# Optimization experiments

Measured on AMD Instinct MI355X. Metric: run time of the kernel, lower is better.

The kernel has to match this reference:

```python
import jax, jax.numpy as jnp
import numpy as np
from jax import lax


def ternarize(w):
    # TWN-style ternarization: threshold delta = 0.7*mean|w|, scale alpha =
    # mean |w| over surviving entries; straight-through in backward.
    aw = jnp.abs(w)
    delta = 0.7 * jnp.mean(aw)
    mask = (aw > delta).astype(w.dtype)
    alpha = jnp.sum(aw * mask) / jnp.maximum(jnp.sum(mask), 1.0)
    q = alpha * jnp.sign(w) * mask
    return w + lax.stop_gradient(q - w)


def conv2d(x, w, b):
    # x: [N,C,H,W], w: [O,I,kh,kw]
    y = lax.conv_general_dilated(x, w, window_strides=(1, 1), padding='VALID',
                                 dimension_numbers=('NCHW', 'OIHW', 'NCHW'))
    return y + b[None, :, None, None]


def maxpool2(x):
    return lax.reduce_window(x, -jnp.inf, lax.max,
                             window_dimensions=(1, 1, 2, 2),
                             window_strides=(1, 1, 2, 2), padding='VALID')


def setup_inputs() -> dict:
    key = jax.random.key(0)
    ks = jax.random.split(key, 11)
    n_classes = 10
    x = jax.random.normal(ks[0], (1024, 1, 32, 32), dtype=jnp.float32)
    # Kaiming-ish scaled params
    w1 = jax.random.normal(ks[1], (32, 1, 5, 5), jnp.float32) * (1.0 / np.sqrt(1 * 25))
    b1 = jnp.zeros((32,), jnp.float32)
    w2 = jax.random.normal(ks[2], (64, 32, 5, 5), jnp.float32) * (1.0 / np.sqrt(32 * 25))
    b2 = jnp.zeros((64,), jnp.float32)
    w3 = jax.random.normal(ks[3], (120, 64, 5, 5), jnp.float32) * (1.0 / np.sqrt(64 * 25))
    b3 = jnp.zeros((120,), jnp.float32)
    fw1 = jax.random.normal(ks[4], (84, 120), jnp.float32) * (1.0 / np.sqrt(120))
    fb1 = jnp.zeros((84,), jnp.float32)
    fw2 = jax.random.normal(ks[5], (n_classes, 84), jnp.float32) * (1.0 / np.sqrt(84))
    fb2 = jnp.zeros((n_classes,), jnp.float32)
    return {"x": x, "w1": w1, "b1": b1, "w2": w2, "b2": b2,
            "w3": w3, "b3": b3, "fw1": fw1, "fb1": fb1, "fw2": fw2, "fb2": fb2}


def reference(x, w1, b1, w2, b2, w3, b3, fw1, fb1, fw2, fb2):
    h = jnp.tanh(conv2d(x, ternarize(w1), b1))   # [N,32,28,28]
    h = maxpool2(h)                              # [N,32,14,14]
    h = jnp.tanh(conv2d(h, ternarize(w2), b2))   # [N,64,10,10]
    h = maxpool2(h)                              # [N,64,5,5]
    h = jnp.tanh(conv2d(h, ternarize(w3), b3))   # [N,120,1,1]
    h = h.reshape(h.shape[0], -1)                # [N,120]
    h = jnp.tanh(h @ ternarize(fw1).T + fb1)     # [N,84]
    logits = h @ ternarize(fw2).T + fb2          # [N,n_classes]
    probs = jax.nn.softmax(logits, axis=1)
    return (logits, probs)
```

## Files before the change

kernel.cpp:

```cpp
#include <hip/hip_runtime.h>
#include <hip/hip_bf16.h>
#include <math.h>


typedef __attribute__((ext_vector_type(8))) short bf16x8;
typedef __attribute__((ext_vector_type(4))) float f32x4;

static const size_t OFF_PB    = 0;
static const size_t OFF_W1B   = 256;
static const size_t OFF_W2B   = 1056;
static const size_t OFF_W3B   = 26656;
static const size_t OFF_FW1T  = 129056;
static const size_t OFF_FW2T  = 139136;
static const size_t OFF_P2B   = 139976;
static const size_t OFF_FLAGS = 959176;

#define BPT 16
#define MAGIC 0x5A17C0DEu

__device__ __forceinline__ ushort f2bf(float v) {
    unsigned u = __float_as_uint(v);
    unsigned r = (u + 0x7FFFu + ((u >> 16) & 1u)) >> 16;
    return (ushort)r;
}
__device__ __forceinline__ float bf2f(ushort h) {
    return __uint_as_float((unsigned)h << 16);
}

__device__ __forceinline__ float tanh_fast(float x) {
    float e = __expf(-2.0f * fabsf(x));
    float r = 1.0f - 2.0f * e / (1.0f + e);
    return copysignf(r, x);
}

__device__ __forceinline__ void tensor_select(int tensor,
        const float* w1, const float* w2, const float* w3,
        const float* fw1, const float* fw2,
        const float*& src, int& O, int& K) {
    switch (tensor) {
        case 0: src = w1;  O = 32;  K = 25;   break;
        case 1: src = w2;  O = 64;  K = 800;  break;
        case 2: src = w3;  O = 120; K = 1600; break;
        case 3: src = fw1; O = 84;  K = 120;  break;
        default: src = fw2; O = 10; K = 84;   break;
    }
}

__device__ __forceinline__ float block_sum_256(float v, float* sbuf) {
    #pragma unroll
    for (int off = 32; off > 0; off >>= 1) v += __shfl_down(v, off);
    const int wid = threadIdx.x >> 6;
    if ((threadIdx.x & 63) == 0) sbuf[wid] = v;
    __syncthreads();
    return sbuf[0] + sbuf[1] + sbuf[2] + sbuf[3];
}

__device__ __forceinline__ float alpha_of(const float* pb, int tensor) {
    float s1 = 0.f, c = 0.f;
    #pragma unroll
    for (int i = 0; i < BPT; ++i) {
        s1 += pb[80 + tensor * BPT + i];
        c  += pb[160 + tensor * BPT + i];
    }
    return s1 / fmaxf(c, 1.0f);
}

__device__ float tern_delta(int tensor, int blk, const float* src, int n,
                            float* pb, unsigned* flags,
                            float* sbuf, float* part) {
    const int t = threadIdx.x;
    float s = 0.f;
    for (int i = blk * 256 + t; i < n; i += BPT * 256) s += fabsf(src[i]);
    s = block_sum_256(s, sbuf);
    if (t == 0) {
        __hip_atomic_store(&pb[tensor * BPT + blk], s,
                           __ATOMIC_RELAXED, __HIP_MEMORY_SCOPE_AGENT);
        __hip_atomic_store(&flags[tensor * BPT + blk], MAGIC,
                           __ATOMIC_RELEASE, __HIP_MEMORY_SCOPE_AGENT);
    }
    if (t < BPT) {
        while (__hip_atomic_load(&flags[tensor * BPT + t],
                                 __ATOMIC_ACQUIRE, __HIP_MEMORY_SCOPE_AGENT)
               != MAGIC) {}
        part[t] = __hip_atomic_load(&pb[tensor * BPT + t],
                                    __ATOMIC_RELAXED, __HIP_MEMORY_SCOPE_AGENT);
    }
    __syncthreads();
    float tot = 0.f;
    #pragma unroll
    for (int i = 0; i < BPT; ++i) tot += part[i];
    return 0.7f * tot / (float)n;
}

__device__ void tern_quantize(int tensor, int blk, const float* src, int n,
                              int O, int K, float delta,
                              ushort* w1b, ushort* w2b, ushort* w3b,
                              float* fw1t, float* fw2t, float* pb,
                              float* sbuf) {
    const int t = threadIdx.x;
    const ushort BP = 0x3F80u, BN = 0xBF80u;
    float s1 = 0.f, cnt = 0.f;

    if (tensor == 0) {
        for (int j = blk * 256 + t; j < 1024; j += BPT * 256) {
            const int oc = j >> 5, kk = j & 31;
            ushort qb = 0;
            if (kk < 25) {
                float w = src[oc * 25 + kk];
                float aw = fabsf(w);
                if (aw > delta) { s1 += aw; cnt += 1.f; qb = (w > 0.f) ? BP : BN; }
            }
            w1b[j] = qb;
        }
    } else if (tensor == 2) {
        for (int i = blk * 256 + t; i < 128 * 1600; i += BPT * 256) {
            ushort qb = 0;
            if (i < n) {
                float w = src[i];
                float aw = fabsf(w);
                if (aw > delta) { s1 += aw; cnt += 1.f; qb = (w > 0.f) ? BP : BN; }
            }
            w3b[i] = qb;
        }
    } else if (tensor == 1) {
        for (int i = blk * 256 + t; i < n; i += BPT * 256) {
            float w = src[i];
            float aw = fabsf(w);
            ushort qb = 0;
            if (aw > delta) { s1 += aw; cnt += 1.f; qb = (w > 0.f) ? BP : BN; }
            int oc = i / 800;
            int r  = i - oc * 800;
            int ic = r / 25;
            int tap = r - ic * 25;
            w2b[oc * 800 + tap * 32 + ic] = qb;
        }
    } else {
        float* dst = (tensor == 3) ? fw1t : fw2t;
        for (int i = blk * 256 + t; i < n; i += BPT * 256) {
            float w = src[i];
            float aw = fabsf(w);
            float q = 0.f;
            if (aw > delta) { s1 += aw; cnt += 1.f; q = (w > 0.f) ? 1.f : -1.f; }
            int o = i / K;
            int k = i - o * K;
            dst[k * O + o] = q;
        }
    }
    __syncthreads();
    s1 = block_sum_256(s1, sbuf);
    __syncthreads();
    cnt = block_sum_256(cnt, sbuf);
    if (t == 0) {
        pb[80 + tensor * BPT + blk]  = s1;
        pb[160 + tensor * BPT + blk] = cnt;
    }
}

__global__ __launch_bounds__(256)
void tern01_kernel(const float* w1, const float* w2,
                   ushort* w1b, ushort* w2b, float* pb, unsigned* flags) {
    __shared__ float sbuf[4];
    __shared__ float part[BPT];
    const int tensor = blockIdx.x >> 4;
    const int blk    = blockIdx.x & 15;
    const float* src; int O, K;
    tensor_select(tensor, w1, w2, nullptr, nullptr, nullptr, src, O, K);
    const int n = O * K;
    const float delta = tern_delta(tensor, blk, src, n, pb, flags, sbuf, part);
    tern_quantize(tensor, blk, src, n, O, K, delta,
                  w1b, w2b, nullptr, nullptr, nullptr, pb, sbuf);
}

#define C2PF 4
__device__ __forceinline__ void conv2_all(
        const ushort* __restrict__ w2b, const ushort* sxt,
        int n0, int mt0, int lane, f32x4 acc[4][2]) {
    const int col = lane & 15, quad = lane >> 4;
    const ushort* abase[4];
    #pragma unroll
    for (int mi = 0; mi < 4; ++mi) {
        int m = (mt0 + mi) * 16 + col;
        m = m < 100 ? m : 99;
        const int pb25 = m >> 2, sub = m & 3;
        const int oh = 2 * (pb25 / 5) + (sub >> 1);
        const int ow = 2 * (pb25 % 5) + (sub & 1);
        abase[mi] = sxt + (oh * 14 + ow) * 40 + quad * 8;
    }
    const ushort* wb0 = w2b + (size_t)(n0 + col) * 800 + quad * 8;
    const ushort* wb1 = wb0 + 16 * 800;
    bf16x8 pb0[C2PF], pb1[C2PF];
    #pragma unroll
    for (int i = 0; i < C2PF; ++i) {
        pb0[i] = *(const bf16x8*)(wb0 + i * 32);
        pb1[i] = *(const bf16x8*)(wb1 + i * 32);
    }
    #pragma unroll
    for (int tap = 0; tap < 25; ++tap) {
        const int slot = tap & (C2PF - 1);
        const bf16x8 b0 = pb0[slot];
        const bf16x8 b1 = pb1[slot];
        if (tap + C2PF < 25) {
            pb0[slot] = *(const bf16x8*)(wb0 + (tap + C2PF) * 32);
            pb1[slot] = *(const bf16x8*)(wb1 + (tap + C2PF) * 32);
        }
        const int kh = tap / 5, kw = tap - kh * 5;
        const int aoff = (kh * 14 + kw) * 40;
        #pragma unroll
        for (int mi = 0; mi < 4; ++mi) {
            bf16x8 af = *(const bf16x8*)(abase[mi] + aoff);
            acc[mi][0] = __builtin_amdgcn_mfma_f32_16x16x32_bf16(af, b0, acc[mi][0], 0, 0, 0);
            acc[mi][1] = __builtin_amdgcn_mfma_f32_16x16x32_bf16(af, b1, acc[mi][1], 0, 0, 0);
        }
    }
}

__global__ __launch_bounds__(256, 4)
void conv12_kernel(const float* __restrict__ x, const ushort* __restrict__ w1b,
                   const float* __restrict__ b1, const ushort* __restrict__ w2b,
                   const float* __restrict__ b2, float* __restrict__ pb,
                   ushort* __restrict__ p2b,
                   const float* __restrict__ w3, const float* __restrict__ fw1,
                   const float* __restrict__ fw2, ushort* __restrict__ w3b,
                   float* __restrict__ fw1t, float* __restrict__ fw2t,
                   unsigned* __restrict__ flags) {
    __shared__ __align__(16) char smem[17744];
    ushort* sxt    = (ushort*)smem;
    ushort* sxb    = (ushort*)(smem + 15680);
    float*  salpha = (float*) (smem + 17728);

    if (blockIdx.x < 48) {
        float* sbuf = (float*)smem;
        float* part = (float*)(smem + 16);
        const int b = blockIdx.x;
        const int tensor = 2 + (b >> 4);
        const int blk = b & 15;
        const float* src; int O, K;
        tensor_select(tensor, nullptr, nullptr, w3, fw1, fw2, src, O, K);
        const int n2 = O * K;
        const float delta = tern_delta(tensor, blk, src, n2, pb, flags, sbuf, part);
        tern_quantize(tensor, blk, src, n2, O, K, delta,
                      nullptr, nullptr, w3b, fw1t, fw2t, pb, sbuf);
        return;
    }

    const int n = blockIdx.x - 48;
    const int t = threadIdx.x;
    const int wave = t >> 6, lane = t & 63;
    const int col = lane & 15, quad = lane >> 4;

    bf16x8 B0 = *(const bf16x8*)(w1b + col * 32 + quad * 8);
    bf16x8 B1 = *(const bf16x8*)(w1b + (col + 16) * 32 + quad * 8);
    const float b1a = b1[col];
    const float b1b = b1[col + 16];

    {
        float4 v = ((const float4*)(x + (size_t)n * 1024))[t];
        ushort4 q;
        q.x = f2bf(v.x); q.y = f2bf(v.y); q.z = f2bf(v.z); q.w = f2bf(v.w);
        *(ushort4*)(sxb + t * 4) = q;
        if (t == 0) salpha[0] = alpha_of(pb, 0);
        if (t == 1) salpha[1] = alpha_of(pb, 1);
    }
    __syncthreads();

    {
        const float a1 = salpha[0];
        const int sub  = col & 3;
        const int colq = col >> 2;
        const int soff = ((sub >> 1) << 5) + (sub & 1);
        int woff[8];
        #pragma unroll
        for (int j = 0; j < 8; ++j) {
            const int tap = quad * 8 + j;
            woff[j] = (tap < 25) ? ((tap / 5) << 5) + (tap % 5) : 0;
        }
        const unsigned kmask = (quad == 3) ? 0u : 0xFFFFFFFFu;

        for (int tl = wave; tl < 49; tl += 4) {
            const int pb4 = tl * 4 + colq;
            const int bh  = (pb4 * 4682) >> 16;
            const int bw  = pb4 - bh * 14;
            const int base = (bh << 6) + (bw << 1) + soff;
            unsigned v0 = sxb[base + woff[0]];
            unsigned v1 = sxb[base + woff[1]] & kmask;
            unsigned v2 = sxb[base + woff[2]] & kmask;
            unsigned v3 = sxb[base + woff[3]] & kmask;
            unsigned v4 = sxb[base + woff[4]] & kmask;
            unsigned v5 = sxb[base + woff[5]] & kmask;
            unsigned v6 = sxb[base + woff[6]] & kmask;
            unsigned v7 = sxb[base + woff[7]] & kmask;
            uint4 u;
            u.x = v0 | (v1 << 16);
            u.y = v2 | (v3 << 16);
            u.z = v4 | (v5 << 16);
            u.w = v6 | (v7 << 16);
            const bf16x8 af = *(const bf16x8*)&u;
            f32x4 z = {};
            f32x4 c0 = __builtin_amdgcn_mfma_f32_16x16x32_bf16(af, B0, z, 0, 0, 0);
            f32x4 c1 = __builtin_amdgcn_mfma_f32_16x16x32_bf16(af, B1, z, 0, 0, 0);
            const int pos2 = tl * 4 + quad;
            const float h01 = bf2f(f2bf(fmaxf(c0[0], c0[1])));
            const float h23 = bf2f(f2bf(fmaxf(c0[2], c0[3])));
            sxt[pos2 * 40 + col] =
                f2bf(tanh_fast(fmaf(a1, fmaxf(h01, h23), b1a)));
            const float g01 = bf2f(f2bf(fmaxf(c1[0], c1[1])));
            const float g23 = bf2f(f2bf(fmaxf(c1[2], c1[3])));
            sxt[pos2 * 40 + col + 16] =
                f2bf(tanh_fast(fmaf(a1, fmaxf(g01, g23), b1b)));
        }
    }
    __syncthreads();

    const int n0  = (wave & 1) * 32;
    const int mt0 = (wave >> 1) * 4;
    f32x4 acc2[4][2] = {};
    conv2_all(w2b, sxt, n0, mt0, lane, acc2);

    {
        const float a2 = salpha[1];
        const float b2a = b2[n0 + col];
        const float b2b = b2[n0 + 16 + col];
        ushort* prow = p2b + (size_t)n * 1600;
        #pragma unroll
        for (int mi = 0; mi < 4; ++mi) {
            const int pb25 = (mt0 + mi) * 4 + quad;
            if (pb25 < 25) {
                #pragma unroll
                for (int np = 0; np < 2; ++np) {
                    const float p01 = fmaxf(acc2[mi][np][0], acc2[mi][np][1]);
                    const float p23 = fmaxf(acc2[mi][np][2], acc2[mi][np][3]);
                    const float pooled = fmaxf(p01, p23);
                    const int oc = n0 + np * 16 + col;
                    const float bb = np ? b2b : b2a;
                    prow[oc * 25 + pb25] =
                        f2bf(tanh_fast(fmaf(a2, pooled, bb)));
                }
            }
        }
    }
}

__global__ __launch_bounds__(1024)
void conv3fc_kernel(const ushort* __restrict__ p2b, const ushort* __restrict__ w3b,
                    const float* __restrict__ b3, const float* __restrict__ pb,
                    const float* __restrict__ fw1t, const float* __restrict__ fb1,
                    const float* __restrict__ fw2t, const float* __restrict__ fb2,
                    float* __restrict__ out) {
    __shared__ __align__(16) char redmem[32768];
    __shared__ __align__(16) float h3s[8][120];
    __shared__ __align__(16) float fw1s[120 * 84];
    __shared__ __align__(16) float fw2s[84 * 10];
    __shared__ float salpha[3];
    float (*red)[8][4][64] = (float (*)[8][4][64])redmem;
    float* sh4 = (float*)redmem;
    float* sl  = (float*)(redmem + 8 * 84 * 4);

    const int t = threadIdx.x;
    const int wave = t >> 6, lane = t & 63;
    const int col = lane & 15, quad = lane >> 4;
    const int img0 = blockIdx.x * 8;
    const int kg  = wave & 3;
    const int ntg = wave >> 2;

    for (int i = t; i < 2520; i += 1024)
        ((float4*)fw1s)[i] = ((const float4*)fw1t)[i];
    if (t < 210) ((float4*)fw2s)[t] = ((const float4*)fw2t)[t];
    if (t == 0) salpha[0] = alpha_of(pb, 2);
    if (t == 1) salpha[1] = alpha_of(pb, 3);
    if (t == 2) salpha[2] = alpha_of(pb, 4);

    const int kstart = (kg < 2) ? kg * 13 : 26 + (kg - 2) * 12;
    const int steps  = (kg < 2) ? 13 : 12;
    const int acol   = (col < 8) ? col : 7;
    const ushort* Abase = p2b + (size_t)(img0 + acol) * 1600 + kstart * 32 + quad * 8;

    f32x4 acc[2] = {};
    {
        const int nt0 = ntg * 2;
        const ushort* Bb0 = w3b + (size_t)(nt0 * 16 + col) * 1600 + kstart * 32 + quad * 8;
        const ushort* Bb1 = Bb0 + (size_t)16 * 1600;
        for (int s = 0; s < steps; ++s) {
            const bf16x8 af = *(const bf16x8*)(Abase + s * 32);
            const bf16x8 b0 = *(const bf16x8*)(Bb0 + s * 32);
            const bf16x8 b1 = *(const bf16x8*)(Bb1 + s * 32);
            acc[0] = __builtin_amdgcn_mfma_f32_16x16x32_bf16(af, b0, acc[0], 0, 0, 0);
            acc[1] = __builtin_amdgcn_mfma_f32_16x16x32_bf16(af, b1, acc[1], 0, 0, 0);
        }
        #pragma unroll
        for (int j = 0; j < 2; ++j)
            #pragma unroll
            for (int r = 0; r < 4; ++r)
                red[kg][nt0 + j][r][lane] = acc[j][r];
    }
    __syncthreads();

    {
        const float a3 = salpha[0];
        const int nt  = t >> 7;
        const int rem = t & 127;
        const int vh  = rem >> 5;
        const int l   = rem & 31;
        const int img = ((l >> 4) << 2) + vh;
        const int oc  = (nt << 4) + (l & 15);
        if (oc < 120) {
            float s = red[0][nt][vh][l] + red[1][nt][vh][l]
                    + red[2][nt][vh][l] + red[3][nt][vh][l];
            h3s[img][oc] = tanh_fast(fmaf(a3, s, b3[oc]));
        }
    }
    __syncthreads();

    if (t < 672) {
        const float af1 = salpha[1];
        const int img = t / 84, oc = t - img * 84;
        float a = 0.f;
        #pragma unroll 4
        for (int k = 0; k < 120; ++k)
            a = fmaf(fw1s[k * 84 + oc], h3s[img][k], a);
        sh4[img * 84 + oc] = tanh_fast(fmaf(af1, a, fb1[oc]));
    }
    __syncthreads();

    if (t < 80) {
        const float af2 = salpha[2];
        const int img = t / 10, oc = t - img * 10;
        float a2 = 0.f;
        #pragma unroll 4
        for (int k = 0; k < 84; ++k)
            a2 = fmaf(fw2s[k * 10 + oc], sh4[img * 84 + k], a2);
        const float lg = fmaf(af2, a2, fb2[oc]);
        sl[img * 10 + oc] = lg;
        out[(size_t)(img0 + img) * 10 + oc] = lg;
    }
    __syncthreads();

    if (t < 80) {
        const int img = t / 10, oc = t - img * 10;
        float m = -INFINITY;
        #pragma unroll
        for (int i = 0; i < 10; ++i) m = fmaxf(m, sl[img * 10 + i]);
        float s = 0.f;
        #pragma unroll
        for (int i = 0; i < 10; ++i) s += expf(sl[img * 10 + i] - m);
        out[10240 + (size_t)(img0 + img) * 10 + oc] = expf(sl[img * 10 + oc] - m) / s;
    }
}

extern "C" void kernel_launch(void* const* d_in, const int* in_sizes, int n_in,
                              void* d_out, int out_size, void* d_ws, size_t ws_size,
                              hipStream_t stream) {
    const float* x   = (const float*)d_in[0];
    const float* w1  = (const float*)d_in[1];
    const float* b1  = (const float*)d_in[2];
    const float* w2  = (const float*)d_in[3];
    const float* b2  = (const float*)d_in[4];
    const float* w3  = (const float*)d_in[5];
    const float* b3  = (const float*)d_in[6];
    const float* fw1 = (const float*)d_in[7];
    const float* fb1 = (const float*)d_in[8];
    const float* fw2 = (const float*)d_in[9];
    const float* fb2 = (const float*)d_in[10];

    float* ws = (float*)d_ws;
    float*    pb    = ws + OFF_PB;
    ushort*   w1b   = (ushort*)(ws + OFF_W1B);
    ushort*   w2b   = (ushort*)(ws + OFF_W2B);
    ushort*   w3b   = (ushort*)(ws + OFF_W3B);
    float*    fw1t  = ws + OFF_FW1T;
    float*    fw2t  = ws + OFF_FW2T;
    ushort*   p2b   = (ushort*)(ws + OFF_P2B);
    unsigned* flags = (unsigned*)(ws + OFF_FLAGS);
    float*    out   = (float*)d_out;

    tern01_kernel<<<32, 256, 0, stream>>>(w1, w2, w1b, w2b, pb, flags);
    conv12_kernel<<<1072, 256, 0, stream>>>(x, w1b, b1, w2b, b2, pb, p2b,
                                            w3, fw1, fw2, w3b, fw1t, fw2t,
                                            flags);
    conv3fc_kernel<<<128, 1024, 0, stream>>>(p2b, w3b, b3, pb,
                                             fw1t, fb1, fw2t, fb2, out);
}
```

Measured before the change: 136.7 us.

## Fold w1/w2 ternarization into conv12 kernel with per-block flag spin-waits

Result: slower. 350.8 us (+156.6%).

```diff
diff --git a/kernel.cpp b/kernel.cpp
--- a/kernel.cpp
+++ b/kernel.cpp
@@ -156,21 +156,6 @@
     }
 }
 
-__global__ __launch_bounds__(256)
-void tern01_kernel(const float* w1, const float* w2,
-                   ushort* w1b, ushort* w2b, float* pb, unsigned* flags) {
-    __shared__ float sbuf[4];
-    __shared__ float part[BPT];
-    const int tensor = blockIdx.x >> 4;
-    const int blk    = blockIdx.x & 15;
-    const float* src; int O, K;
-    tensor_select(tensor, w1, w2, nullptr, nullptr, nullptr, src, O, K);
-    const int n = O * K;
-    const float delta = tern_delta(tensor, blk, src, n, pb, flags, sbuf, part);
-    tern_quantize(tensor, blk, src, n, O, K, delta,
-                  w1b, w2b, nullptr, nullptr, nullptr, pb, sbuf);
-}
-
 #define C2PF 4
 __device__ __forceinline__ void conv2_all(
         const ushort* __restrict__ w2b, const ushort* sxt,
@@ -215,38 +200,55 @@
 }
 
 __global__ __launch_bounds__(256, 4)
-void conv12_kernel(const float* __restrict__ x, const ushort* __restrict__ w1b,
-                   const float* __restrict__ b1, const ushort* __restrict__ w2b,
-                   const float* __restrict__ b2, float* __restrict__ pb,
-                   ushort* __restrict__ p2b,
+void conv12_kernel(const float* __restrict__ x,
+                   const float* __restrict__ w1, const float* __restrict__ w2,
                    const float* __restrict__ w3, const float* __restrict__ fw1,
-                   const float* __restrict__ fw2, ushort* __restrict__ w3b,
-                   float* __restrict__ fw1t, float* __restrict__ fw2t,
-                   unsigned* __restrict__ flags) {
+                   const float* __restrict__ fw2,
+                   const float* __restrict__ b1, const float* __restrict__ b2,
+                   float* __restrict__ pb, ushort* __restrict__ p2b,
+                   ushort* __restrict__ w1b, ushort* __restrict__ w2b,
+                   ushort* __restrict__ w3b, float* __restrict__ fw1t,
+                   float* __restrict__ fw2t, unsigned* __restrict__ flags) {
     __shared__ __align__(16) char smem[17744];
     ushort* sxt    = (ushort*)smem;
     ushort* sxb    = (ushort*)(smem + 15680);
     float*  salpha = (float*) (smem + 17728);
 
-    if (blockIdx.x < 48) {
+    const int t = threadIdx.x;
+
+    if (blockIdx.x < 80) {
         float* sbuf = (float*)smem;
         float* part = (float*)(smem + 16);
         const int b = blockIdx.x;
-        const int tensor = 2 + (b >> 4);
+        const int tensor = b >> 4;
         const int blk = b & 15;
         const float* src; int O, K;
-        tensor_select(tensor, nullptr, nullptr, w3, fw1, fw2, src, O, K);
+        tensor_select(tensor, w1, w2, w3, fw1, fw2, src, O, K);
         const int n2 = O * K;
         const float delta = tern_delta(tensor, blk, src, n2, pb, flags, sbuf, part);
         tern_quantize(tensor, blk, src, n2, O, K, delta,
-                      nullptr, nullptr, w3b, fw1t, fw2t, pb, sbuf);
+                      w1b, w2b, w3b, fw1t, fw2t, pb, sbuf);
+        __syncthreads();
+        if (t == 0) {
+            __threadfence();
+            __hip_atomic_store(&flags[80 + tensor * BPT + blk], MAGIC,
+                               __ATOMIC_RELEASE, __HIP_MEMORY_SCOPE_AGENT);
+        }
         return;
     }
 
-    const int n = blockIdx.x - 48;
-    const int t = threadIdx.x;
+    const int n = blockIdx.x - 80;
     const int wave = t >> 6, lane = t & 63;
     const int col = lane & 15, quad = lane >> 4;
+
+    if (t < BPT) {
+        while (__hip_atomic_load(&flags[80 + t],
+                                 __ATOMIC_ACQUIRE, __HIP_MEMORY_SCOPE_AGENT)
+               != MAGIC)
+            __builtin_amdgcn_s_sleep(8);
+        __threadfence();
+    }
+    __syncthreads();
 
     bf16x8 B0 = *(const bf16x8*)(w1b + col * 32 + quad * 8);
     bf16x8 B1 = *(const bf16x8*)(w1b + (col + 16) * 32 + quad * 8);
@@ -259,7 +261,6 @@
         q.x = f2bf(v.x); q.y = f2bf(v.y); q.z = f2bf(v.z); q.w = f2bf(v.w);
         *(ushort4*)(sxb + t * 4) = q;
         if (t == 0) salpha[0] = alpha_of(pb, 0);
-        if (t == 1) salpha[1] = alpha_of(pb, 1);
     }
     __syncthreads();
 
@@ -311,6 +312,17 @@
     }
     __syncthreads();
 
+    if (t < BPT) {
+        while (__hip_atomic_load(&flags[80 + BPT + t],
+                                 __ATOMIC_ACQUIRE, __HIP_MEMORY_SCOPE_AGENT)
+               != MAGIC)
+            __builtin_amdgcn_s_sleep(8);
+        __threadfence();
+    }
+    __syncthreads();
+    if (t == 0) salpha[1] = alpha_of(pb, 1);
+    __syncthreads();
+
     const int n0  = (wave & 1) * 32;
     const int mt0 = (wave >> 1) * 4;
     f32x4 acc2[4][2] = {};
@@ -472,10 +484,9 @@
     unsigned* flags = (unsigned*)(ws + OFF_FLAGS);
     float*    out   = (float*)d_out;
 
-    tern01_kernel<<<32, 256, 0, stream>>>(w1, w2, w1b, w2b, pb, flags);
-    conv12_kernel<<<1072, 256, 0, stream>>>(x, w1b, b1, w2b, b2, pb, p2b,
-                                            w3, fw1, fw2, w3b, fw1t, fw2t,
-                                            flags);
+    conv12_kernel<<<1104, 256, 0, stream>>>(x, w1, w2, w3, fw1, fw2, b1, b2,
+                                            pb, p2b, w1b, w2b, w3b, fw1t,
+                                            fw2t, flags);
     conv3fc_kernel<<<128, 1024, 0, stream>>>(p2b, w3b, b3, pb,
                                              fw1t, fb1, fw2t, fb2, out);
 }
```
